# Kernel optimization log

Measured on AMD Instinct MI355X. Metric: run time of the kernel, lower is better.

The kernel has to match this reference:

```python
import jax, jax.numpy as jnp
import numpy as np


def _gcn(x, src, dst, W, b, n):
    # PyG GCNConv: out = D^-1/2 (A+I) D^-1/2 (x @ W) + b, deg includes self-loop
    xw = x @ W
    ones = jnp.ones(src.shape[0], x.dtype)
    deg = jax.ops.segment_sum(ones, dst, num_segments=n) + 1.0
    dinv = jax.lax.rsqrt(deg)
    norm = (dinv[src] * dinv[dst])[:, None]
    agg = jax.ops.segment_sum(xw[src] * norm, dst, num_segments=n)
    agg = agg + xw / deg[:, None]  # self-loop term: norm = 1/deg
    return agg + b


def _bn(x, g, b, m, v, eps=1e-5):
    # BatchNorm1d eval mode with running stats
    return (x - m) * jax.lax.rsqrt(v + eps) * g + b


def setup_inputs() -> dict:
    key = jax.random.key(0)
    ks = jax.random.split(key, 32)
    N, E, G, F, H, D, L, EM = 500000, 2500000, 10000, 64, 64, 128, 10, 160000
    s = 0.05
    inp = {
        'x': jax.random.normal(ks[0], (N, F), jnp.float32),
        'edge_index': jax.random.randint(ks[1], (2, E), 0, N),
        'batch': jnp.sort(jax.random.randint(ks[2], (N,), 0, G)),
        'macro_edges': jax.random.randint(ks[3], (2, EM), 0, G),
        'G': G,
        'W1': jax.random.normal(ks[4], (F, H)) * s, 'b1': jnp.zeros((H,)),
        'W2': jax.random.normal(ks[5], (H, H)) * s, 'b2': jnp.zeros((H,)),
        'FW1': jax.random.normal(ks[6], (H, D)) * s, 'Fb1': jnp.zeros((D,)),
        'FW2': jax.random.normal(ks[7], (D, L)) * s, 'Fb2': jnp.zeros((L,)),
        'MW1': jax.random.normal(ks[8], (D, D)) * s, 'mb1': jnp.zeros((D,)),
        'g1': jnp.ones((D,)), 'be1': jnp.zeros((D,)),
        'm1': jnp.zeros((D,)), 'v1': jnp.ones((D,)),
        'MW2': jax.random.normal(ks[9], (D, D)) * s, 'mb2': jnp.zeros((D,)),
        'g2': jnp.ones((D,)), 'be2': jnp.zeros((D,)),
        'm2': jnp.zeros((D,)), 'v2': jnp.ones((D,)),
        'MW3': jax.random.normal(ks[10], (D, L)) * s, 'mb3': jnp.zeros((L,)),
    }
    return inp


def reference(x, edge_index, batch, macro_edges, G,
              W1, b1, W2, b2, FW1, Fb1, FW2, Fb2,
              MW1, mb1, g1, be1, m1, v1,
              MW2, mb2, g2, be2, m2, v2,
              MW3, mb3):
    n = x.shape[0]
    src, dst = edge_index[0], edge_index[1]
    # SAGE (graph-level model), eval mode => dropout is identity
    h1 = jax.nn.relu(_gcn(x, src, dst, W1, b1, n))
    h2 = jax.nn.relu(_gcn(h1, src, dst, W2, b2, n))
    a1 = h2 @ FW1 + Fb1
    sums = jax.ops.segment_sum(a1, batch, num_segments=G)
    cnt = jax.ops.segment_sum(jnp.ones(n, x.dtype), batch, num_segments=G)
    loc = sums / jnp.maximum(cnt, 1.0)[:, None]        # [G, 128] graph embeddings
    ic = loc @ FW2 + Fb2                                # [G, L]
    # SuperMacroGCN over macro graph
    ms, md = macro_edges[0], macro_edges[1]
    z = jax.nn.relu(_bn(_gcn(loc, ms, md, MW1, mb1, G), g1, be1, m1, v1))
    z = jax.nn.relu(_bn(_gcn(z, ms, md, MW2, mb2, G), g2, be2, m2, v2))
    glob = z
    hc = _gcn(glob, ms, md, MW3, mb3, G)
    return (hc, ic, loc, glob, jnp.float32(0.0))
```

## Files before the change

### kernel.cpp

```cpp
#include <hip/hip_runtime.h>
#include <hip/hip_fp16.h>


typedef float nf4 __attribute__((ext_vector_type(4)));
typedef _Float16 v4h __attribute__((ext_vector_type(4)));
typedef float v4f __attribute__((ext_vector_type(4)));
struct __align__(8) h4 { __half2 a, b; };

__global__ void hist_kernel(const int* __restrict__ dst, int* __restrict__ hist, int E) {
    int e = blockIdx.x * blockDim.x + threadIdx.x;
    if (e < E) atomicAdd(&hist[dst[e]], 1);
}

__global__ void finalize_deg(const int* __restrict__ hist, float* __restrict__ dinv,
                             float* __restrict__ drecip, int n) {
    int i = blockIdx.x * blockDim.x + threadIdx.x;
    if (i < n) {
        float c = (float)hist[i] + 1.0f;
        dinv[i]   = rsqrtf(c);
        drecip[i] = 1.0f / c;
    }
}

__global__ void gcnt_kernel(const int* __restrict__ batch, float* __restrict__ invc,
                            float* __restrict__ bscale, int N, int G) {
    int g = blockIdx.x * blockDim.x + threadIdx.x;
    if (g >= G) return;
    int lo = 0, hi = N;
    while (lo < hi) { int m = (lo + hi) >> 1; if (batch[m] < g) lo = m + 1; else hi = m; }
    int s = lo;
    hi = N;
    while (lo < hi) { int m = (lo + hi) >> 1; if (batch[m] < g + 1) lo = m + 1; else hi = m; }
    int cnt = lo - s;
    invc[g]   = (cnt > 0) ? 1.f / (float)cnt : 0.f;
    bscale[g] = (cnt > 0) ? 1.f : 0.f;
}

__global__ __launch_bounds__(256) void scan1(const int* __restrict__ cnt, int* __restrict__ pre,
                                             int* __restrict__ bsum, int n) {
    __shared__ int s[256];
    int base = blockIdx.x * 1024;
    int t = threadIdx.x;
    int v[4];
    int loc = 0;
#pragma unroll
    for (int j = 0; j < 4; j++) {
        int i = base + t * 4 + j;
        v[j] = (i < n) ? cnt[i] : 0;
        loc += v[j];
    }
    s[t] = loc;
    __syncthreads();
    for (int off = 1; off < 256; off <<= 1) {
        int x = (t >= off) ? s[t - off] : 0;
        __syncthreads();
        s[t] += x;
        __syncthreads();
    }
    int run = s[t] - loc;
    if (t == 255) bsum[blockIdx.x] = s[255];
#pragma unroll
    for (int j = 0; j < 4; j++) {
        int i = base + t * 4 + j;
        if (i < n) pre[i] = run;
        run += v[j];
    }
}

__global__ __launch_bounds__(512) void scan2(int* __restrict__ bsum, int nb) {
    __shared__ int s[512];
    int t = threadIdx.x;
    int v = (t < nb) ? bsum[t] : 0;
    s[t] = v;
    __syncthreads();
    for (int off = 1; off < 512; off <<= 1) {
        int x = (t >= off) ? s[t - off] : 0;
        __syncthreads();
        s[t] += x;
        __syncthreads();
    }
    if (t < nb) bsum[t] = s[t] - v;
}

__global__ void scan3(int* __restrict__ pre, const int* __restrict__ bsum,
                      int* __restrict__ cursor, int n, int E) {
    int i = blockIdx.x * blockDim.x + threadIdx.x;
    if (i < n) {
        int v = pre[i] + bsum[i >> 10];
        pre[i] = v;
        cursor[i] = v;
    }
    if (i == 0) pre[n] = E;
}

__global__ __launch_bounds__(256) void scatter_xcd(const int* __restrict__ src,
                                                   const int* __restrict__ dst,
                                                   int* __restrict__ cursor,
                                                   int* __restrict__ col,
                                                   int E, int per_chunk, int npx) {
    int bucket = blockIdx.x & 7;
    int chunk  = blockIdx.x >> 3;
    int lo = bucket * npx;
    int hi = lo + npx;
    int e0 = chunk * per_chunk;
    int e1 = min(e0 + per_chunk, E);
    for (int e = e0 + threadIdx.x; e < e1; e += 256) {
        int d = dst[e];
        if (d < lo || d >= hi) continue;
        int p = atomicAdd(&cursor[d], 1);
        col[p] = src[e];
    }
}

__global__ void scatter_kernel(const int* __restrict__ src, const int* __restrict__ dst,
                               int* __restrict__ cursor, int* __restrict__ col, int E) {
    int e = blockIdx.x * blockDim.x + threadIdx.x;
    if (e >= E) return;
    int p = atomicAdd(&cursor[dst[e]], 1);
    col[p] = src[e];
}

__global__ __launch_bounds__(256) void csr_agg_bn128(const int* __restrict__ rowptr,
                                                     const int* __restrict__ col,
                                                     const float* __restrict__ A,
                                                     const float* __restrict__ bias,
                                                     const float* __restrict__ dinv,
                                                     const float* __restrict__ gam,
                                                     const float* __restrict__ bet,
                                                     const float* __restrict__ mean,
                                                     const float* __restrict__ var,
                                                     float* __restrict__ Z, int N) {
    constexpr int F = 128, TPN = 32, NPB = 8;
    int node = blockIdx.x * NPB + threadIdx.x / TPN;
    int lane = threadIdx.x % TPN;
    if (node >= N) return;
    int c = lane * 4;
    float4 acc = *(const float4*)&A[(size_t)node * F + c];
    int e0 = rowptr[node], e1 = rowptr[node + 1];
    int e = e0;
    for (; e + 4 <= e1; e += 4) {
        int s0 = col[e + 0], s1 = col[e + 1], s2 = col[e + 2], s3 = col[e + 3];
        float4 v0 = *(const float4*)&A[(size_t)s0 * F + c];
        float4 v1 = *(const float4*)&A[(size_t)s1 * F + c];
        float4 v2 = *(const float4*)&A[(size_t)s2 * F + c];
        float4 v3 = *(const float4*)&A[(size_t)s3 * F + c];
        acc.x += v0.x + v1.x + v2.x + v3.x;
        acc.y += v0.y + v1.y + v2.y + v3.y;
        acc.z += v0.z + v1.z + v2.z + v3.z;
        acc.w += v0.w + v1.w + v2.w + v3.w;
    }
    for (; e < e1; e++) {
        int s = col[e];
        float4 v = *(const float4*)&A[(size_t)s * F + c];
        acc.x += v.x; acc.y += v.y; acc.z += v.z; acc.w += v.w;
    }
    float dv = dinv[node];
    float4 b4 = *(const float4*)&bias[c];
    float4 g4 = *(const float4*)&gam[c];
    float4 be4 = *(const float4*)&bet[c];
    float4 m4 = *(const float4*)&mean[c];
    float4 v4 = *(const float4*)&var[c];
    float4 o;
    o.x = fmaxf((acc.x * dv + b4.x - m4.x) * rsqrtf(v4.x + 1e-5f) * g4.x + be4.x, 0.f);
    o.y = fmaxf((acc.y * dv + b4.y - m4.y) * rsqrtf(v4.y + 1e-5f) * g4.y + be4.y, 0.f);
    o.z = fmaxf((acc.z * dv + b4.z - m4.z) * rsqrtf(v4.z + 1e-5f) * g4.z + be4.z, 0.f);
    o.w = fmaxf((acc.w * dv + b4.w - m4.w) * rsqrtf(v4.w + 1e-5f) * g4.w + be4.w, 0.f);
    *(float4*)&Z[(size_t)node * F + c] = o;
}

__global__ __launch_bounds__(256) void gemm_n64(const float* __restrict__ X,
                                                const float* __restrict__ W,
                                                const float* __restrict__ dinv,
                                                __half* __restrict__ XW, int N) {
    __shared__ float Xs[64][68];
    const int tid = threadIdx.x;
    const int tc = tid & 15;
    const int tr = tid >> 4;
    const int r0 = blockIdx.x * 64;

#pragma unroll
    for (int p = 0; p < 4; p++) {
        int row = p * 16 + (tid >> 4);
        int col = (tid & 15) * 4;
        float4 v = make_float4(0.f, 0.f, 0.f, 0.f);
        if (r0 + row < N) {
            nf4 nv = __builtin_nontemporal_load((const nf4*)&X[(size_t)(r0 + row) * 64 + col]);
            v = make_float4(nv.x, nv.y, nv.z, nv.w);
        }
        *(float4*)&Xs[row][col] = v;
    }
    __syncthreads();

    float acc[4][4];
#pragma unroll
    for (int i = 0; i < 4; i++)
#pragma unroll
        for (int j = 0; j < 4; j++) acc[i][j] = 0.f;

    const float* wp = W + tc * 4;
#pragma unroll 8
    for (int k = 0; k < 64; k++) {
        float4 wv = *(const float4*)&wp[k * 64];
        float x0 = Xs[tr * 4 + 0][k];
        float x1 = Xs[tr * 4 + 1][k];
        float x2 = Xs[tr * 4 + 2][k];
        float x3 = Xs[tr * 4 + 3][k];
        acc[0][0] += x0 * wv.x; acc[0][1] += x0 * wv.y; acc[0][2] += x0 * wv.z; acc[0][3] += x0 * wv.w;
        acc[1][0] += x1 * wv.x; acc[1][1] += x1 * wv.y; acc[1][2] += x1 * wv.z; acc[1][3] += x1 * wv.w;
        acc[2][0] += x2 * wv.x; acc[2][1] += x2 * wv.y; acc[2][2] += x2 * wv.z; acc[2][3] += x2 * wv.w;
        acc[3][0] += x3 * wv.x; acc[3][1] += x3 * wv.y; acc[3][2] += x3 * wv.z; acc[3][3] += x3 * wv.w;
    }

#pragma unroll
    for (int i = 0; i < 4; i++) {
        int row = r0 + tr * 4 + i;
        if (row >= N) continue;
        float dv = dinv[row];
        h4 o;
        o.a = __floats2half2_rn(acc[i][0] * dv, acc[i][1] * dv);
        o.b = __floats2half2_rn(acc[i][2] * dv, acc[i][3] * dv);
        *(h4*)&XW[(size_t)row * 64 + tc * 4] = o;
    }
}

__global__ __launch_bounds__(256) void gemm_agg_n64(const int* __restrict__ rowptr,
                                                    const int* __restrict__ col,
                                                    const __half* __restrict__ A,
                                                    const float* __restrict__ b_prev,
                                                    const float* __restrict__ W,
                                                    const float* __restrict__ dinv,
                                                    __half* __restrict__ XW, int N) {
    __shared__ _Float16 Xh[64][68];
    __shared__ _Float16 WhT[64][68];
    const int tid = threadIdx.x;
    const int r0 = blockIdx.x * 64;

    for (int i = tid; i < 4096; i += 256) {
        int k = i >> 6, c = i & 63;
        WhT[c][k] = (_Float16)W[i];
    }

#pragma unroll
    for (int p = 0; p < 4; p++) {
        int row = p * 16 + (tid >> 4);
        int node = r0 + row;
        int c = (tid & 15) * 4;
        float4 acc = make_float4(0.f, 0.f, 0.f, 0.f);
        if (node < N) {
            h4 sv = *(const h4*)&A[(size_t)node * 64 + c];
            float2 f0 = __half22float2(sv.a);
            float2 f1 = __half22float2(sv.b);
            acc = make_float4(f0.x, f0.y, f1.x, f1.y);
            int e0 = rowptr[node], e1 = rowptr[node + 1];
            int e = e0;
            for (; e + 4 <= e1; e += 4) {
                int s0 = col[e + 0], s1 = col[e + 1], s2 = col[e + 2], s3 = col[e + 3];
                h4 v0 = *(const h4*)&A[(size_t)s0 * 64 + c];
                h4 v1 = *(const h4*)&A[(size_t)s1 * 64 + c];
                h4 v2 = *(const h4*)&A[(size_t)s2 * 64 + c];
                h4 v3 = *(const h4*)&A[(size_t)s3 * 64 + c];
                float2 a0 = __half22float2(v0.a), b0 = __half22float2(v0.b);
                float2 a1 = __half22float2(v1.a), b1 = __half22float2(v1.b);
                float2 a2 = __half22float2(v2.a), b2 = __half22float2(v2.b);
                float2 a3 = __half22float2(v3.a), b3 = __half22float2(v3.b);
                acc.x += a0.x + a1.x + a2.x + a3.x;
                acc.y += a0.y + a1.y + a2.y + a3.y;
                acc.z += b0.x + b1.x + b2.x + b3.x;
                acc.w += b0.y + b1.y + b2.y + b3.y;
            }
            for (; e < e1; e++) {
                int s = col[e];
                h4 v = *(const h4*)&A[(size_t)s * 64 + c];
                float2 a = __half22float2(v.a), b = __half22float2(v.b);
                acc.x += a.x; acc.y += a.y; acc.z += b.x; acc.w += b.y;
            }
            float dv = dinv[node];
            float4 b4 = *(const float4*)&b_prev[c];
            acc.x = fmaxf(acc.x * dv + b4.x, 0.f);
            acc.y = fmaxf(acc.y * dv + b4.y, 0.f);
            acc.z = fmaxf(acc.z * dv + b4.z, 0.f);
            acc.w = fmaxf(acc.w * dv + b4.w, 0.f);
        }
        v4h o;
        o.x = (_Float16)acc.x; o.y = (_Float16)acc.y;
        o.z = (_Float16)acc.z; o.w = (_Float16)acc.w;
        *(v4h*)&Xh[row][c] = o;
    }
    __syncthreads();

    const int wv = tid >> 6;
    const int lane = tid & 63;
    const int lr = lane & 15;
    const int kg = lane >> 4;

    v4f acc0 = {0.f, 0.f, 0.f, 0.f};
    v4f acc1 = {0.f, 0.f, 0.f, 0.f};
    v4f acc2 = {0.f, 0.f, 0.f, 0.f};
    v4f acc3 = {0.f, 0.f, 0.f, 0.f};
#pragma unroll
    for (int s = 0; s < 4; s++) {
        v4h af = *(const v4h*)&Xh[wv * 16 + lr][s * 16 + kg * 4];
        v4h bf0 = *(const v4h*)&WhT[0 * 16 + lr][s * 16 + kg * 4];
        v4h bf1 = *(const v4h*)&WhT[1 * 16 + lr][s * 16 + kg * 4];
        v4h bf2 = *(const v4h*)&WhT[2 * 16 + lr][s * 16 + kg * 4];
        v4h bf3 = *(const v4h*)&WhT[3 * 16 + lr][s * 16 + kg * 4];
        acc0 = __builtin_amdgcn_mfma_f32_16x16x16f16(af, bf0, acc0, 0, 0, 0);
        acc1 = __builtin_amdgcn_mfma_f32_16x16x16f16(af, bf1, acc1, 0, 0, 0);
        acc2 = __builtin_amdgcn_mfma_f32_16x16x16f16(af, bf2, acc2, 0, 0, 0);
        acc3 = __builtin_amdgcn_mfma_f32_16x16x16f16(af, bf3, acc3, 0, 0, 0);
    }

#pragma unroll
    for (int j = 0; j < 4; j++) {
        int row = r0 + wv * 16 + kg * 4 + j;
        if (row >= N) continue;
        float dv = dinv[row];
        XW[(size_t)row * 64 +  0 + lr] = (__half)(acc0[j] * dv);
        XW[(size_t)row * 64 + 16 + lr] = (__half)(acc1[j] * dv);
        XW[(size_t)row * 64 + 32 + lr] = (__half)(acc2[j] * dv);
        XW[(size_t)row * 64 + 48 + lr] = (__half)(acc3[j] * dv);
    }
}

__global__ __launch_bounds__(256) void segmean_agg(const int* __restrict__ rowptr,
                                                   const int* __restrict__ col,
                                                   const __half* __restrict__ A2,
                                                   const float* __restrict__ b2,
                                                   const float* __restrict__ dinv,
                                                   const int* __restrict__ batch,
                                                   const float* __restrict__ invc,
                                                   float* __restrict__ M, int N) {
    __shared__ float Xs[64][68];
    __shared__ int gb[64];
    const int tid = threadIdx.x;
    const int r0 = blockIdx.x * 64;

    if (tid < 64) gb[tid] = (r0 + tid < N) ? batch[r0 + tid] : -1;

#pragma unroll
    for (int p = 0; p < 4; p++) {
        int row = p * 16 + (tid >> 4);
        int node = r0 + row;
        int c = (tid & 15) * 4;
        float4 acc = make_float4(0.f, 0.f, 0.f, 0.f);
        if (node < N) {
            h4 sv = *(const h4*)&A2[(size_t)node * 64 + c];
            float2 f0 = __half22float2(sv.a);
            float2 f1 = __half22float2(sv.b);
            acc = make_float4(f0.x, f0.y, f1.x, f1.y);
            int e0 = rowptr[node], e1 = rowptr[node + 1];
            int e = e0;
            for (; e + 4 <= e1; e += 4) {
                int s0 = col[e + 0], s1 = col[e + 1], s2 = col[e + 2], s3 = col[e + 3];
                h4 v0 = *(const h4*)&A2[(size_t)s0 * 64 + c];
                h4 v1 = *(const h4*)&A2[(size_t)s1 * 64 + c];
                h4 v2 = *(const h4*)&A2[(size_t)s2 * 64 + c];
                h4 v3 = *(const h4*)&A2[(size_t)s3 * 64 + c];
                float2 a0 = __half22float2(v0.a), q0 = __half22float2(v0.b);
                float2 a1 = __half22float2(v1.a), q1 = __half22float2(v1.b);
                float2 a2 = __half22float2(v2.a), q2 = __half22float2(v2.b);
                float2 a3 = __half22float2(v3.a), q3 = __half22float2(v3.b);
                acc.x += a0.x + a1.x + a2.x + a3.x;
                acc.y += a0.y + a1.y + a2.y + a3.y;
                acc.z += q0.x + q1.x + q2.x + q3.x;
                acc.w += q0.y + q1.y + q2.y + q3.y;
            }
            for (; e < e1; e++) {
                int s = col[e];
                h4 v = *(const h4*)&A2[(size_t)s * 64 + c];
                float2 a = __half22float2(v.a), q = __half22float2(v.b);
                acc.x += a.x; acc.y += a.y; acc.z += q.x; acc.w += q.y;
            }
            float dv = dinv[node];
            float4 b4 = *(const float4*)&b2[c];
            acc.x = fmaxf(acc.x * dv + b4.x, 0.f);
            acc.y = fmaxf(acc.y * dv + b4.y, 0.f);
            acc.z = fmaxf(acc.z * dv + b4.z, 0.f);
            acc.w = fmaxf(acc.w * dv + b4.w, 0.f);
        }
        *(float4*)&Xs[row][c] = acc;
    }
    __syncthreads();

    if (tid < 64) {
        int t = tid;
        float run = 0.f;
        int curg = gb[0];
        for (int r = 0; r < 64; r++) {
            int g2 = gb[r];
            if (g2 != curg) {
                if (curg >= 0) atomicAdd(&M[(size_t)curg * 64 + t], run * invc[curg]);
                run = 0.f;
                curg = g2;
            }
            if (g2 >= 0) run += Xs[r][t];
        }
        if (curg >= 0) atomicAdd(&M[(size_t)curg * 64 + t], run * invc[curg]);
    }
}

__global__ __launch_bounds__(256) void loc_gemm(const float* __restrict__ M,
                                                const float* __restrict__ FW1,
                                                const float* __restrict__ Fb1,
                                                const float* __restrict__ bscale,
                                                float* __restrict__ loc, int G) {
    __shared__ float Xs[64][68];
    __shared__ float Ws[64][64];
    __shared__ float bs[64];
    const int tid = threadIdx.x;
    const int tc = tid & 15;
    const int tr = tid >> 4;
    const int r0 = blockIdx.x * 64;
    const int c0 = blockIdx.y * 64;

    for (int i = tid; i < 4096; i += 256)
        Ws[i >> 6][i & 63] = FW1[(size_t)(i >> 6) * 128 + c0 + (i & 63)];
    if (tid < 64) bs[tid] = Fb1[c0 + tid];
#pragma unroll
    for (int p = 0; p < 4; p++) {
        int row = p * 16 + (tid >> 4);
        int col = (tid & 15) * 4;
        float4 v = make_float4(0.f, 0.f, 0.f, 0.f);
        if (r0 + row < G) v = *(const float4*)&M[(size_t)(r0 + row) * 64 + col];
        *(float4*)&Xs[row][col] = v;
    }
    __syncthreads();

    float acc[4][4];
#pragma unroll
    for (int i = 0; i < 4; i++)
#pragma unroll
        for (int j = 0; j < 4; j++) acc[i][j] = 0.f;

#pragma unroll 8
    for (int k = 0; k < 64; k++) {
        float4 wv = *(const float4*)&Ws[k][tc * 4];
        float x0 = Xs[tr * 4 + 0][k];
        float x1 = Xs[tr * 4 + 1][k];
        float x2 = Xs[tr * 4 + 2][k];
        float x3 = Xs[tr * 4 + 3][k];
        acc[0][0] += x0 * wv.x; acc[0][1] += x0 * wv.y; acc[0][2] += x0 * wv.z; acc[0][3] += x0 * wv.w;
        acc[1][0] += x1 * wv.x; acc[1][1] += x1 * wv.y; acc[1][2] += x1 * wv.z; acc[1][3] += x1 * wv.w;
        acc[2][0] += x2 * wv.x; acc[2][1] += x2 * wv.y; acc[2][2] += x2 * wv.z; acc[2][3] += x2 * wv.w;
        acc[3][0] += x3 * wv.x; acc[3][1] += x3 * wv.y; acc[3][2] += x3 * wv.z; acc[3][3] += x3 * wv.w;
    }

#pragma unroll
    for (int i = 0; i < 4; i++) {
        int row = r0 + tr * 4 + i;
        if (row >= G) continue;
        float sc = bscale[row];
        float4 o;
        o.x = acc[i][0] + sc * bs[tc * 4 + 0];
        o.y = acc[i][1] + sc * bs[tc * 4 + 1];
        o.z = acc[i][2] + sc * bs[tc * 4 + 2];
        o.w = acc[i][3] + sc * bs[tc * 4 + 3];
        *(float4*)&loc[(size_t)row * 128 + c0 + tc * 4] = o;
    }
}

__global__ __launch_bounds__(256) void ic_kernel(const float* __restrict__ loc,
                                                 const float* __restrict__ FW2,
                                                 const float* __restrict__ Fb2,
                                                 float* __restrict__ ic,
                                                 float* __restrict__ scalar_out, int G) {
    __shared__ float Ws[1280];
    __shared__ float bs[10];
    for (int i = threadIdx.x; i < 1280; i += 256) Ws[i] = FW2[i];
    if (threadIdx.x < 10) bs[threadIdx.x] = Fb2[threadIdx.x];
    __syncthreads();
    int g = blockIdx.x * 256 + threadIdx.x;
    if (g == 0) scalar_out[0] = 0.f;
    if (g >= G) return;
    float acc[10];
#pragma unroll
    for (int j = 0; j < 10; j++) acc[j] = bs[j];
    const float* xr = loc + (size_t)g * 128;
    for (int k = 0; k < 128; k++) {
        float xv = xr[k];
#pragma unroll
        for (int j = 0; j < 10; j++) acc[j] += xv * Ws[k * 10 + j];
    }
    float* o = ic + (size_t)g * 10;
#pragma unroll
    for (int j = 0; j < 10; j++) o[j] = acc[j];
}

__global__ __launch_bounds__(256) void gemm_g128(const float* __restrict__ X,
                                                 const float* __restrict__ W,
                                                 const float* __restrict__ dinv,
                                                 float* __restrict__ ZW, int G) {
    __shared__ float Xs[64][68];
    __shared__ float Ws[64][64];
    const int tid = threadIdx.x;
    const int tc = tid & 15;
    const int tr = tid >> 4;
    const int r0 = blockIdx.x * 64;
    const int c0 = blockIdx.y * 64;

    float acc[4][4];
#pragma unroll
    for (int i = 0; i < 4; i++)
#pragma unroll
        for (int j = 0; j < 4; j++) acc[i][j] = 0.f;

    for (int kc = 0; kc < 2; kc++) {
        __syncthreads();
        for (int i = tid; i < 4096; i += 256)
            Ws[i >> 6][i & 63] = W[(size_t)(kc * 64 + (i >> 6)) * 128 + c0 + (i & 63)];
#pragma unroll
        for (int p = 0; p < 4; p++) {
            int row = p * 16 + (tid >> 4);
            int col = (tid & 15) * 4;
            float4 v = make_float4(0.f, 0.f, 0.f, 0.f);
            if (r0 + row < G) v = *(const float4*)&X[(size_t)(r0 + row) * 128 + kc * 64 + col];
            *(float4*)&Xs[row][col] = v;
        }
        __syncthreads();
#pragma unroll 8
        for (int k = 0; k < 64; k++) {
            float4 wv = *(const float4*)&Ws[k][tc * 4];
            float x0 = Xs[tr * 4 + 0][k];
            float x1 = Xs[tr * 4 + 1][k];
            float x2 = Xs[tr * 4 + 2][k];
            float x3 = Xs[tr * 4 + 3][k];
            acc[0][0] += x0 * wv.x; acc[0][1] += x0 * wv.y; acc[0][2] += x0 * wv.z; acc[0][3] += x0 * wv.w;
            acc[1][0] += x1 * wv.x; acc[1][1] += x1 * wv.y; acc[1][2] += x1 * wv.z; acc[1][3] += x1 * wv.w;
            acc[2][0] += x2 * wv.x; acc[2][1] += x2 * wv.y; acc[2][2] += x2 * wv.z; acc[2][3] += x2 * wv.w;
            acc[3][0] += x3 * wv.x; acc[3][1] += x3 * wv.y; acc[3][2] += x3 * wv.z; acc[3][3] += x3 * wv.w;
        }
    }

#pragma unroll
    for (int i = 0; i < 4; i++) {
        int row = r0 + tr * 4 + i;
        if (row >= G) continue;
        float dv = dinv[row];
        *(float4*)&ZW[(size_t)row * 128 + c0 + tc * 4] =
            make_float4(acc[i][0] * dv, acc[i][1] * dv, acc[i][2] * dv, acc[i][3] * dv);
    }
}

__global__ __launch_bounds__(256) void gemm_g10(const float* __restrict__ X,
                                                const float* __restrict__ W,
                                                const float* __restrict__ bias,
                                                const float* __restrict__ mdrecip,
                                                float* __restrict__ ZW,
                                                float* __restrict__ HC, int G) {
    __shared__ float Ws[1280];
    __shared__ float bs[10];
    for (int i = threadIdx.x; i < 1280; i += 256) Ws[i] = W[i];
    if (threadIdx.x < 10) bs[threadIdx.x] = bias[threadIdx.x];
    __syncthreads();
    int g = blockIdx.x * 256 + threadIdx.x;
    if (g >= G) return;
    float acc[10];
#pragma unroll
    for (int j = 0; j < 10; j++) acc[j] = 0.f;
    const float4* xr = (const float4*)(X + (size_t)g * 128);
#pragma unroll 4
    for (int k4 = 0; k4 < 32; k4++) {
        float4 v = xr[k4];
        float xv[4] = {v.x, v.y, v.z, v.w};
#pragma unroll
        for (int d = 0; d < 4; d++) {
            float xs = xv[d];
            int k = k4 * 4 + d;
#pragma unroll
            for (int j = 0; j < 10; j++) acc[j] += xs * Ws[k * 10 + j];
        }
    }
    float dr = mdrecip[g];
    float* zw = ZW + (size_t)g * 10;
    float* hc = HC + (size_t)g * 10;
#pragma unroll
    for (int j = 0; j < 10; j++) {
        zw[j] = acc[j];
        hc[j] = acc[j] * dr + bs[j];
    }
}

__global__ void edge_agg10(const int* __restrict__ ms, const int* __restrict__ md,
                           const float* __restrict__ mdinv, const float* __restrict__ ZW,
                           float* __restrict__ HC, int EM) {
    int e = blockIdx.x * blockDim.x + threadIdx.x;
    if (e >= EM) return;
    int s = ms[e], d = md[e];
    float w = mdinv[s] * mdinv[d];
    const float* zr = ZW + (size_t)s * 10;
    float* out = HC + (size_t)d * 10;
#pragma unroll
    for (int j = 0; j < 10; j++) atomicAdd(out + j, zr[j] * w);
}

extern "C" void kernel_launch(void* const* d_in, const int* in_sizes, int n_in,
                              void* d_out, int out_size, void* d_ws, size_t ws_size,
                              hipStream_t stream) {
    const float* x    = (const float*)d_in[0];
    const int*   ei   = (const int*)d_in[1];
    const int*   batch= (const int*)d_in[2];
    const int*   me   = (const int*)d_in[3];
    const float* W1   = (const float*)d_in[5];
    const float* b1   = (const float*)d_in[6];
    const float* W2   = (const float*)d_in[7];
    const float* b2   = (const float*)d_in[8];
    const float* FW1  = (const float*)d_in[9];
    const float* Fb1  = (const float*)d_in[10];
    const float* FW2  = (const float*)d_in[11];
    const float* Fb2  = (const float*)d_in[12];
    const float* MW1  = (const float*)d_in[13];
    const float* mb1  = (const float*)d_in[14];
    const float* g1   = (const float*)d_in[15];
    const float* be1  = (const float*)d_in[16];
    const float* m1   = (const float*)d_in[17];
    const float* v1   = (const float*)d_in[18];
    const float* MW2  = (const float*)d_in[19];
    const float* mb2  = (const float*)d_in[20];
    const float* g2   = (const float*)d_in[21];
    const float* be2  = (const float*)d_in[22];
    const float* m2   = (const float*)d_in[23];
    const float* v2   = (const float*)d_in[24];
    const float* MW3  = (const float*)d_in[25];
    const float* mb3  = (const float*)d_in[26];

    const int N  = in_sizes[0] / 64;
    const int E  = in_sizes[1] / 2;
    const int EM = in_sizes[3] / 2;
    const int G  = (out_size - 1) / 276;

    float* out    = (float*)d_out;
    float* hc     = out;
    float* ic     = out + (size_t)G * 10;
    float* loc    = out + (size_t)G * 20;
    float* glob   = out + (size_t)G * 20 + (size_t)G * 128;
    float* scalar = out + (size_t)G * 276;

    char*  ws  = (char*)d_ws;
    size_t off = 0;
    auto alloc = [&](size_t bytes) -> void* {
        void* p = (void*)(ws + off);
        off += (bytes + 255) & ~(size_t)255;
        return p;
    };
    int*    hist    = (int*)alloc((size_t)(N + 1) * 4);
    int*    rowptr  = (int*)alloc((size_t)(N + 1) * 4);
    int*    cursor  = (int*)alloc((size_t)N * 4);
    int*    bsum    = (int*)alloc(512 * 4);
    int*    col     = (int*)alloc((size_t)E * 4);
    float*  dinv    = (float*)alloc((size_t)N * 4);
    float*  drecip  = (float*)alloc((size_t)N * 4);
    int*    mhist   = (int*)alloc((size_t)(G + 1) * 4);
    int*    mrowptr = (int*)alloc((size_t)(G + 1) * 4);
    int*    mcursor = (int*)alloc((size_t)G * 4);
    int*    mbsum   = (int*)alloc(512 * 4);
    int*    mcol    = (int*)alloc((size_t)EM * 4);
    float*  mdinv   = (float*)alloc((size_t)G * 4);
    float*  mdrecip = (float*)alloc((size_t)G * 4);
    __half* A       = (__half*)alloc((size_t)N * 64 * 2);
    __half* A2      = (__half*)alloc((size_t)N * 64 * 2);
    float*  M       = (float*)alloc((size_t)G * 64 * 4);
    float*  invc    = (float*)alloc((size_t)G * 4);
    float*  bscale  = (float*)alloc((size_t)G * 4);
    float*  mzw     = (float*)alloc((size_t)G * 128 * 4);
    float*  z1      = (float*)alloc((size_t)G * 128 * 4);
    float*  zw3     = (float*)alloc((size_t)G * 10 * 4);
    (void)ws_size;

    const int* src = ei;
    const int* dst = ei + E;
    const int* ms  = me;
    const int* md  = me + EM;

    hipMemsetAsync(hist, 0, (size_t)(N + 1) * 4, stream);
    hipMemsetAsync(mhist, 0, (size_t)(G + 1) * 4, stream);
    hipMemsetAsync(M, 0, (size_t)G * 64 * 4, stream);
    hist_kernel<<<(E + 255) / 256, 256, 0, stream>>>(dst, hist, E);
    hist_kernel<<<(EM + 255) / 256, 256, 0, stream>>>(md, mhist, EM);
    finalize_deg<<<(N + 255) / 256, 256, 0, stream>>>(hist, dinv, drecip, N);
    finalize_deg<<<(G + 255) / 256, 256, 0, stream>>>(mhist, mdinv, mdrecip, G);
    gcnt_kernel<<<(G + 255) / 256, 256, 0, stream>>>(batch, invc, bscale, N, G);

    const int nb1 = (N + 1023) / 1024;
    scan1<<<nb1, 256, 0, stream>>>(hist, rowptr, bsum, N);
    scan2<<<1, 512, 0, stream>>>(bsum, nb1);
    scan3<<<(N + 255) / 256, 256, 0, stream>>>(rowptr, bsum, cursor, N, E);
    const int nb2 = (G + 1023) / 1024;
    scan1<<<nb2, 256, 0, stream>>>(mhist, mrowptr, mbsum, G);
    scan2<<<1, 512, 0, stream>>>(mbsum, nb2);
    scan3<<<(G + 255) / 256, 256, 0, stream>>>(mrowptr, mbsum, mcursor, G, EM);

    {
        const int nchunks = 2048;
        const int per_chunk = (E + nchunks - 1) / nchunks;
        const int npx = (N + 7) / 8;
        scatter_xcd<<<nchunks * 8, 256, 0, stream>>>(src, dst, cursor, col, E, per_chunk, npx);
    }
    scatter_kernel<<<(EM + 255) / 256, 256, 0, stream>>>(ms, md, mcursor, mcol, EM);

    const int nblk = (N + 63) / 64;

    gemm_n64<<<nblk, 256, 0, stream>>>(x, W1, dinv, A, N);
    gemm_agg_n64<<<nblk, 256, 0, stream>>>(rowptr, col, A, b1, W2, dinv, A2, N);
    segmean_agg<<<nblk, 256, 0, stream>>>(rowptr, col, A2, b2, dinv, batch, invc, M, N);
    {
        dim3 lg((G + 63) / 64, 2);
        loc_gemm<<<lg, 256, 0, stream>>>(M, FW1, Fb1, bscale, loc, G);
    }
    ic_kernel<<<(G + 255) / 256, 256, 0, stream>>>(loc, FW2, Fb2, ic, scalar, G);

    dim3 mg((G + 63) / 64, 2);

    gemm_g128<<<mg, 256, 0, stream>>>(loc, MW1, mdinv, mzw, G);
    csr_agg_bn128<<<(G * 32 + 255) / 256, 256, 0, stream>>>(mrowptr, mcol, mzw, mb1, mdinv,
                                                            g1, be1, m1, v1, z1, G);
    gemm_g128<<<mg, 256, 0, stream>>>(z1, MW2, mdinv, mzw, G);
    csr_agg_bn128<<<(G * 32 + 255) / 256, 256, 0, stream>>>(mrowptr, mcol, mzw, mb2, mdinv,
                                                            g2, be2, m2, v2, glob, G);

    gemm_g10<<<(G + 255) / 256, 256, 0, stream>>>(glob, MW3, mb3, mdrecip, zw3, hc, G);
    edge_agg10<<<(EM + 255) / 256, 256, 0, stream>>>(ms, md, mdinv, zw3, hc, EM);
}
```

Measured before the change: 705.9 us.

## Build CSR via two-pass binning with bucket atomics then LDS-local scatter

Replaces the per-node global-atomic scatter with a two-stage counting sort. Edges are first binned into 256-node buckets, with one global atomic per edge on a small bucket-cursor array, and written as (src,dst) pairs. A second kernel then places each bucket's edges into col using shared-memory atomics. The aim is to cut random global atomics and scattered writes, at the cost of an extra E*8-byte pair buffer and an extra pass over it.

```diff
diff --git a/kernel.cpp b/kernel.cpp
--- a/kernel.cpp
+++ b/kernel.cpp
@@ -93,22 +93,45 @@
     if (i == 0) pre[n] = E;
 }
 
-__global__ __launch_bounds__(256) void scatter_xcd(const int* __restrict__ src,
-                                                   const int* __restrict__ dst,
-                                                   int* __restrict__ cursor,
-                                                   int* __restrict__ col,
-                                                   int E, int per_chunk, int npx) {
-    int bucket = blockIdx.x & 7;
-    int chunk  = blockIdx.x >> 3;
-    int lo = bucket * npx;
-    int hi = lo + npx;
+__global__ void init_bcur(const int* __restrict__ rowptr, int* __restrict__ bcur, int NB) {
+    int k = blockIdx.x * blockDim.x + threadIdx.x;
+    if (k < NB) bcur[k] = rowptr[k << 8];
+}
+
+__global__ __launch_bounds__(256) void bin_edges(const int* __restrict__ src,
+                                                 const int* __restrict__ dst,
+                                                 int* __restrict__ bcur,
+                                                 int2* __restrict__ pairs,
+                                                 int E, int per_chunk) {
+    int xg = blockIdx.x & 7;
+    int chunk = blockIdx.x >> 3;
     int e0 = chunk * per_chunk;
     int e1 = min(e0 + per_chunk, E);
     for (int e = e0 + threadIdx.x; e < e1; e += 256) {
         int d = dst[e];
-        if (d < lo || d >= hi) continue;
-        int p = atomicAdd(&cursor[d], 1);
-        col[p] = src[e];
+        int k = d >> 8;
+        if ((k & 7) != xg) continue;
+        int p = atomicAdd(&bcur[k], 1);
+        pairs[p] = make_int2(src[e], d);
+    }
+}
+
+__global__ __launch_bounds__(256) void build_col(const int* __restrict__ rowptr,
+                                                 const int2* __restrict__ pairs,
+                                                 int* __restrict__ col, int N) {
+    __shared__ int lcur[256];
+    int k = blockIdx.x;
+    int n0 = k << 8;
+    int n1 = min(n0 + 256, N);
+    int tid = threadIdx.x;
+    if (n0 + tid < n1) lcur[tid] = rowptr[n0 + tid];
+    __syncthreads();
+    int pBase = rowptr[n0];
+    int pEnd  = rowptr[n1];
+    for (int i = pBase + tid; i < pEnd; i += 256) {
+        int2 pr = pairs[i];
+        int p = atomicAdd(&lcur[pr.y - n0], 1);
+        col[p] = pr.x;
     }
 }
 
@@ -642,11 +665,15 @@
         off += (bytes + 255) & ~(size_t)255;
         return p;
     };
+    const int NB = (N + 255) >> 8;
+
     int*    hist    = (int*)alloc((size_t)(N + 1) * 4);
     int*    rowptr  = (int*)alloc((size_t)(N + 1) * 4);
     int*    cursor  = (int*)alloc((size_t)N * 4);
     int*    bsum    = (int*)alloc(512 * 4);
     int*    col     = (int*)alloc((size_t)E * 4);
+    int2*   pairs   = (int2*)alloc((size_t)E * 8);
+    int*    bcur    = (int*)alloc((size_t)NB * 4);
     float*  dinv    = (float*)alloc((size_t)N * 4);
     float*  drecip  = (float*)alloc((size_t)N * 4);
     int*    mhist   = (int*)alloc((size_t)(G + 1) * 4);
@@ -689,12 +716,13 @@
     scan2<<<1, 512, 0, stream>>>(mbsum, nb2);
     scan3<<<(G + 255) / 256, 256, 0, stream>>>(mrowptr, mbsum, mcursor, G, EM);
 
+    init_bcur<<<(NB + 255) / 256, 256, 0, stream>>>(rowptr, bcur, NB);
     {
-        const int nchunks = 2048;
+        const int nchunks = 1024;
         const int per_chunk = (E + nchunks - 1) / nchunks;
-        const int npx = (N + 7) / 8;
-        scatter_xcd<<<nchunks * 8, 256, 0, stream>>>(src, dst, cursor, col, E, per_chunk, npx);
-    }
+        bin_edges<<<nchunks * 8, 256, 0, stream>>>(src, dst, bcur, pairs, E, per_chunk);
+    }
+    build_col<<<NB, 256, 0, stream>>>(rowptr, pairs, col, N);
     scatter_kernel<<<(EM + 255) / 256, 256, 0, stream>>>(ms, md, mcursor, mcol, EM);
 
     const int nblk = (N + 63) / 64;
```

Measured after the change: 1.004 ms. 42.2% more time.
